# Kernel optimization log

Hardware: AMD Instinct MI355X
Metric: run time of the kernel (lower is better)

## Reference

```python
import jax, jax.numpy as jnp
import numpy as np

HEAD_DIM = 128
N_LAYERS = 32


def setup_inputs() -> dict:
    key = jax.random.key(0)
    kx, kk, kv = jax.random.split(key, 3)
    x = jax.random.normal(kx, (1, 32, 1, HEAD_DIM), dtype=jnp.float32)       # [B,H,1,D] single decode token
    k = jax.random.normal(kk, (1, 32, 8192, HEAD_DIM), dtype=jnp.float32)    # [B,H,S,D] key cache
    v = jax.random.normal(kv, (1, 32, 8192, HEAD_DIM), dtype=jnp.float32)    # [B,H,S,D] value cache
    return {"x": x, "k": k, "v": v}


def _decode_attn(x, k, v):
    # x: [B,H,1,D], k/v: [B,H,S,D]
    scale = 1.0 / np.sqrt(HEAD_DIM).astype(np.float32)
    scores = jnp.einsum("bhqd,bhsd->bhqs", x, k) * scale   # [B,H,1,S]
    probs = jax.nn.softmax(scores, axis=-1)
    return jnp.einsum("bhqs,bhsd->bhqd", probs, v)          # [B,H,1,D]


def reference(x, k, v):
    # gen_id is the (static) cache length; 32 layered decode steps share the cache,
    # mirroring the original loop over 32 layers.
    for _ in range(N_LAYERS):
        x = _decode_attn(x, k, v)
    return (k, v, x)
```

## Files before the change

### kernel.cpp

```cpp
#include <hip/hip_runtime.h>
#include <math.h>

#define HEAD_DIM 128
#define NHEADS   32
#define SLEN     8192
#define NLAYERS  32
#define KROW     (SLEN / 2)
#define VROW     (HEAD_DIM / 2)

#define SPLITS   16
#define CHUNK    (SLEN / SPLITS)
#define PSTR     132
#define SCALE    0.088388347648318447f

typedef unsigned int   uint;
typedef unsigned char  uchar;
typedef __attribute__((ext_vector_type(2))) float f2v;

__device__ __forceinline__ f2v d4_0(uint w) { return __builtin_amdgcn_cvt_scalef32_pk_f32_fp4(w, 1.0f, 0); }
__device__ __forceinline__ f2v d4_1(uint w) { return __builtin_amdgcn_cvt_scalef32_pk_f32_fp4(w, 1.0f, 1); }
__device__ __forceinline__ f2v d4_2(uint w) { return __builtin_amdgcn_cvt_scalef32_pk_f32_fp4(w, 1.0f, 2); }
__device__ __forceinline__ f2v d4_3(uint w) { return __builtin_amdgcn_cvt_scalef32_pk_f32_fp4(w, 1.0f, 3); }

__device__ __forceinline__ uint pk8_fp4(float a0, float a1, float a2, float a3,
                                        float a4, float a5, float a6, float a7) {
    uint r = 0;
    r = __builtin_amdgcn_cvt_scalef32_pk_fp4_f32(r, a0, a1, 1.0f, 0);
    r = __builtin_amdgcn_cvt_scalef32_pk_fp4_f32(r, a2, a3, 1.0f, 1);
    r = __builtin_amdgcn_cvt_scalef32_pk_fp4_f32(r, a4, a5, 1.0f, 2);
    r = __builtin_amdgcn_cvt_scalef32_pk_fp4_f32(r, a6, a7, 1.0f, 3);
    return r;
}

template<bool WRITE_OUT>
__global__ __launch_bounds__(256)
void convert_kT(const float* __restrict__ k, uchar* __restrict__ kbt,
                float* __restrict__ kout)
{
    const int h   = blockIdx.x >> 7;
    const int st  = blockIdx.x & 127;
    const int tid = threadIdx.x;

    __shared__ float tile[HEAD_DIM][65];

    const int   srow0 = tid >> 5;
    const int   c4    = (tid & 31) * 4;
    const size_t kbase = ((size_t)h * SLEN + (size_t)st * 64) * HEAD_DIM;

    #pragma unroll
    for (int it = 0; it < 8; ++it) {
        const int s = srow0 + it * 8;
        const float4 v = *(const float4*)(k + kbase + (size_t)s * HEAD_DIM + c4);
        if (WRITE_OUT) *(float4*)(kout + kbase + (size_t)s * HEAD_DIM + c4) = v;
        tile[c4 + 0][s] = v.x; tile[c4 + 1][s] = v.y;
        tile[c4 + 2][s] = v.z; tile[c4 + 3][s] = v.w;
    }
    __syncthreads();

    const int d0  = tid >> 3;
    const int sl8 = (tid & 7) * 8;
    #pragma unroll
    for (int it = 0; it < 4; ++it) {
        const int d = d0 + it * 32;
        const uint u = pk8_fp4(tile[d][sl8 + 0], tile[d][sl8 + 1],
                               tile[d][sl8 + 2], tile[d][sl8 + 3],
                               tile[d][sl8 + 4], tile[d][sl8 + 5],
                               tile[d][sl8 + 6], tile[d][sl8 + 7]);
        *(uint*)(kbt + ((size_t)h * HEAD_DIM + d) * KROW + st * 32 + (tid & 7) * 4) = u;
    }
}

template<bool WRITE_OUT>
__global__ void convert_v(const float4* __restrict__ v, uint2* __restrict__ vb,
                          float4* __restrict__ vout, size_t n16)
{
    size_t i = (size_t)blockIdx.x * blockDim.x + threadIdx.x;
    const size_t stride = (size_t)gridDim.x * blockDim.x;
    for (size_t j = i; j < n16; j += stride) {
        const float4 b0 = v[4 * j], b1 = v[4 * j + 1], b2 = v[4 * j + 2], b3 = v[4 * j + 3];
        if (WRITE_OUT) {
            vout[4 * j] = b0; vout[4 * j + 1] = b1;
            vout[4 * j + 2] = b2; vout[4 * j + 3] = b3;
        }
        uint2 p;
        p.x = pk8_fp4(b0.x, b0.y, b0.z, b0.w, b1.x, b1.y, b1.z, b1.w);
        p.y = pk8_fp4(b2.x, b2.y, b2.z, b2.w, b3.x, b3.y, b3.z, b3.w);
        vb[j] = p;
    }
}

__global__ void copy_kv(const float4* __restrict__ k, const float4* __restrict__ v,
                        float4* __restrict__ out, size_t n4)
{
    size_t i = (size_t)blockIdx.x * blockDim.x + threadIdx.x;
    const size_t stride = (size_t)gridDim.x * blockDim.x;
    for (size_t j = i; j < n4; j += stride) {
        out[j]      = k[j];
        out[n4 + j] = v[j];
    }
}

__global__ __launch_bounds__(512)
void attn_layer(const float* __restrict__ x0,
                const float* __restrict__ part_in,
                const uchar* __restrict__ kbt,
                const uchar* __restrict__ vb,
                float* __restrict__ part_out)
{
    const int h    = blockIdx.x >> 4;
    const int sp   = blockIdx.x & 15;
    const int tid  = threadIdx.x;
    const int lane = tid & 63;
    const int w    = tid >> 6;

    __shared__ float xs[HEAD_DIM];
    __shared__ float sc[CHUNK];
    __shared__ float scpv[8][HEAD_DIM];
    __shared__ float lred[8];
    __shared__ float xpart[2][HEAD_DIM + 1];
    __shared__ float lpro[2];

    if (part_in) {
        const float* __restrict__ ph = part_in + (size_t)h * SPLITS * PSTR;
        if (tid < 256) {
            const int d = tid & 127, g = tid >> 7;
            float a = 0.f;
            #pragma unroll
            for (int i = 0; i < 8; ++i)
                a += ph[(size_t)(g * 8 + i) * PSTR + 1 + d];
            xpart[g][d] = a;
        } else if (tid < 258) {
            const int g = tid - 256;
            float l = 0.f;
            #pragma unroll
            for (int i = 0; i < 8; ++i)
                l += ph[(size_t)(g * 8 + i) * PSTR];
            lpro[g] = l;
        }
        __syncthreads();
        if (tid < HEAD_DIM)
            xs[tid] = (xpart[0][tid] + xpart[1][tid]) / (lpro[0] + lpro[1]) * SCALE;
    } else {
        if (tid < HEAD_DIM) xs[tid] = x0[h * HEAD_DIM + tid] * SCALE;
    }
    __syncthreads();

    const int sgrp = lane & 3;
    const int dgrp = lane >> 2;
    const uchar* __restrict__ kh = kbt + (size_t)h * HEAD_DIM * KROW + (size_t)sp * (CHUNK / 2);
    const int sboff = w * 32 + sgrp * 8;
    float a16[16];
    #pragma unroll
    for (int j = 0; j < 16; ++j) a16[j] = 0.f;
    #pragma unroll
    for (int it = 0; it < 8; ++it) {
        const int d = it * 16 + dgrp;
        const uint2 kk = *(const uint2*)(kh + (size_t)d * KROW + sboff);
        const float xd = xs[d];
        f2v t;
        t = d4_0(kk.x); a16[0]  = fmaf(t.x, xd, a16[0]);  a16[1]  = fmaf(t.y, xd, a16[1]);
        t = d4_1(kk.x); a16[2]  = fmaf(t.x, xd, a16[2]);  a16[3]  = fmaf(t.y, xd, a16[3]);
        t = d4_2(kk.x); a16[4]  = fmaf(t.x, xd, a16[4]);  a16[5]  = fmaf(t.y, xd, a16[5]);
        t = d4_3(kk.x); a16[6]  = fmaf(t.x, xd, a16[6]);  a16[7]  = fmaf(t.y, xd, a16[7]);
        t = d4_0(kk.y); a16[8]  = fmaf(t.x, xd, a16[8]);  a16[9]  = fmaf(t.y, xd, a16[9]);
        t = d4_1(kk.y); a16[10] = fmaf(t.x, xd, a16[10]); a16[11] = fmaf(t.y, xd, a16[11]);
        t = d4_2(kk.y); a16[12] = fmaf(t.x, xd, a16[12]); a16[13] = fmaf(t.y, xd, a16[13]);
        t = d4_3(kk.y); a16[14] = fmaf(t.x, xd, a16[14]); a16[15] = fmaf(t.y, xd, a16[15]);
    }
    #pragma unroll
    for (int j = 0; j < 16; ++j) {
        a16[j] += __shfl_xor(a16[j], 4);
        a16[j] += __shfl_xor(a16[j], 8);
        a16[j] += __shfl_xor(a16[j], 16);
        a16[j] += __shfl_xor(a16[j], 32);
    }
    float lp = 0.f;
    if (dgrp == 0) {
        const int base = w * 64 + sgrp * 16;
        #pragma unroll
        for (int j = 0; j < 16; ++j) { a16[j] = __expf(a16[j]); lp += a16[j]; }
        #pragma unroll
        for (int j = 0; j < 16; j += 4)
            *(float4*)&sc[base + j] = make_float4(a16[j], a16[j+1], a16[j+2], a16[j+3]);
    }
    #pragma unroll
    for (int off = 1; off < 64; off <<= 1)
        lp += __shfl_xor(lp, off);
    if (lane == 0) lred[w] = lp;
    __syncthreads();

    const int rg = tid >> 3;
    const int dg = tid & 7;
    const uchar* __restrict__ vg = vb + ((size_t)h * SLEN + (size_t)sp * CHUNK) * VROW;
    float acc[16];
    #pragma unroll
    for (int j = 0; j < 16; ++j) acc[j] = 0.f;
    #pragma unroll
    for (int it = 0; it < 8; ++it) {
        const int s1 = rg + it * 64;
        const uint2 vv = *(const uint2*)(vg + (size_t)s1 * VROW + dg * 8);
        const float pp = sc[s1];
        f2v t;
        t = d4_0(vv.x); acc[0]  = fmaf(pp, t.x, acc[0]);  acc[1]  = fmaf(pp, t.y, acc[1]);
        t = d4_1(vv.x); acc[2]  = fmaf(pp, t.x, acc[2]);  acc[3]  = fmaf(pp, t.y, acc[3]);
        t = d4_2(vv.x); acc[4]  = fmaf(pp, t.x, acc[4]);  acc[5]  = fmaf(pp, t.y, acc[5]);
        t = d4_3(vv.x); acc[6]  = fmaf(pp, t.x, acc[6]);  acc[7]  = fmaf(pp, t.y, acc[7]);
        t = d4_0(vv.y); acc[8]  = fmaf(pp, t.x, acc[8]);  acc[9]  = fmaf(pp, t.y, acc[9]);
        t = d4_1(vv.y); acc[10] = fmaf(pp, t.x, acc[10]); acc[11] = fmaf(pp, t.y, acc[11]);
        t = d4_2(vv.y); acc[12] = fmaf(pp, t.x, acc[12]); acc[13] = fmaf(pp, t.y, acc[13]);
        t = d4_3(vv.y); acc[14] = fmaf(pp, t.x, acc[14]); acc[15] = fmaf(pp, t.y, acc[15]);
    }
    #pragma unroll
    for (int j = 0; j < 16; ++j) {
        acc[j] += __shfl_xor(acc[j], 8);
        acc[j] += __shfl_xor(acc[j], 16);
        acc[j] += __shfl_xor(acc[j], 32);
    }
    if (lane < 8) {
        #pragma unroll
        for (int j = 0; j < 16; j += 4)
            *(float4*)&scpv[w][lane * 16 + j] = make_float4(acc[j], acc[j+1], acc[j+2], acc[j+3]);
    }
    __syncthreads();

    float* __restrict__ po = part_out + ((size_t)h * SPLITS + sp) * PSTR;
    if (tid < HEAD_DIM) {
        float a = 0.f;
        #pragma unroll
        for (int g = 0; g < 8; ++g) a += scpv[g][tid];
        po[1 + tid] = a;
    }
    if (tid == 0) {
        float Ls = 0.f;
        #pragma unroll
        for (int i = 0; i < 8; ++i) Ls += lred[i];
        po[0] = Ls;
    }
}

__global__ __launch_bounds__(128)
void attn_combine(const float* __restrict__ part, float* __restrict__ xout)
{
    const float* __restrict__ ph = part + (size_t)blockIdx.x * SPLITS * PSTR;
    float a = 0.f, l = 0.f;
    #pragma unroll
    for (int i = 0; i < SPLITS; ++i) {
        a += ph[(size_t)i * PSTR + 1 + threadIdx.x];
        l += ph[(size_t)i * PSTR];
    }
    xout[blockIdx.x * HEAD_DIM + threadIdx.x] = a / l;
}

extern "C" void kernel_launch(void* const* d_in, const int* in_sizes, int n_in,
                              void* d_out, int out_size, void* d_ws, size_t ws_size,
                              hipStream_t stream)
{
    const float* x = (const float*)d_in[0];
    const float* k = (const float*)d_in[1];
    const float* v = (const float*)d_in[2];
    float* out = (float*)d_out;

    const size_t kvN = (size_t)NHEADS * SLEN * HEAD_DIM;
    const size_t partElems = (size_t)NHEADS * SPLITS * PSTR;

    float* part0 = (float*)d_ws;
    float* part1 = part0 + partElems;

    const size_t needWs = 2 * partElems * sizeof(float) + kvN;
    uchar* kbt;
    uchar* vb;
    const bool ws_path = (ws_size >= needWs + 256);
    if (ws_path) kbt = (uchar*)(part1 + partElems);
    else         kbt = (uchar*)out;
    vb = kbt + kvN / 2;

    if (ws_path) {
        convert_kT<true><<<NHEADS * 128, 256, 0, stream>>>(k, kbt, out);
        convert_v<true><<<2048, 256, 0, stream>>>(
            (const float4*)v, (uint2*)vb, (float4*)(out + kvN), kvN / 16);
    } else {
        convert_kT<false><<<NHEADS * 128, 256, 0, stream>>>(k, kbt, nullptr);
        convert_v<false><<<2048, 256, 0, stream>>>(
            (const float4*)v, (uint2*)vb, nullptr, kvN / 16);
    }

    for (int layer = 0; layer < NLAYERS; ++layer) {
        float* pout = (layer & 1) ? part1 : part0;
        const float* pin = (layer == 0) ? nullptr : ((layer & 1) ? part0 : part1);
        attn_layer<<<NHEADS * SPLITS, 512, 0, stream>>>(
            (layer == 0) ? x : nullptr, pin, kbt, vb, pout);
    }
    attn_combine<<<NHEADS, 128, 0, stream>>>(part1, out + 2 * kvN);

    if (!ws_path) {
        copy_kv<<<2048, 256, 0, stream>>>((const float4*)k, (const float4*)v,
                                          (float4*)out, kvN / 4);
    }
}
```

Baseline: 472.9 us.

## Split QK dot-product across warps by head dim, reduce partial scores in LDS

```diff
diff --git a/kernel.cpp b/kernel.cpp
--- a/kernel.cpp
+++ b/kernel.cpp
@@ -11,6 +11,7 @@
 #define SPLITS   16
 #define CHUNK    (SLEN / SPLITS)
 #define PSTR     132
+#define SCP_STR  20
 #define SCALE    0.088388347648318447f
 
 typedef unsigned int   uint;
@@ -114,6 +115,7 @@
     const int w    = tid >> 6;
 
     __shared__ float xs[HEAD_DIM];
+    __shared__ float scp[8][32 * SCP_STR];
     __shared__ float sc[CHUNK];
     __shared__ float scpv[8][HEAD_DIM];
     __shared__ float lred[8];
@@ -145,17 +147,16 @@
     }
     __syncthreads();
 
-    const int sgrp = lane & 3;
-    const int dgrp = lane >> 2;
+    const int dpar = lane >> 5;
+    const int sgp  = lane & 31;
     const uchar* __restrict__ kh = kbt + (size_t)h * HEAD_DIM * KROW + (size_t)sp * (CHUNK / 2);
-    const int sboff = w * 32 + sgrp * 8;
     float a16[16];
     #pragma unroll
     for (int j = 0; j < 16; ++j) a16[j] = 0.f;
     #pragma unroll
     for (int it = 0; it < 8; ++it) {
-        const int d = it * 16 + dgrp;
-        const uint2 kk = *(const uint2*)(kh + (size_t)d * KROW + sboff);
+        const int d = it * 16 + (w << 1) + dpar;
+        const uint2 kk = *(const uint2*)(kh + (size_t)d * KROW + sgp * 8);
         const float xd = xs[d];
         f2v t;
         t = d4_0(kk.x); a16[0]  = fmaf(t.x, xd, a16[0]);  a16[1]  = fmaf(t.y, xd, a16[1]);
@@ -168,25 +169,25 @@
         t = d4_3(kk.y); a16[14] = fmaf(t.x, xd, a16[14]); a16[15] = fmaf(t.y, xd, a16[15]);
     }
     #pragma unroll
-    for (int j = 0; j < 16; ++j) {
-        a16[j] += __shfl_xor(a16[j], 4);
-        a16[j] += __shfl_xor(a16[j], 8);
-        a16[j] += __shfl_xor(a16[j], 16);
-        a16[j] += __shfl_xor(a16[j], 32);
-    }
-    float lp = 0.f;
-    if (dgrp == 0) {
-        const int base = w * 64 + sgrp * 16;
-        #pragma unroll
-        for (int j = 0; j < 16; ++j) { a16[j] = __expf(a16[j]); lp += a16[j]; }
+    for (int j = 0; j < 16; ++j) a16[j] += __shfl_xor(a16[j], 32);
+    if (lane < 32) {
         #pragma unroll
         for (int j = 0; j < 16; j += 4)
-            *(float4*)&sc[base + j] = make_float4(a16[j], a16[j+1], a16[j+2], a16[j+3]);
-    }
+            *(float4*)&scp[w][sgp * SCP_STR + j] =
+                make_float4(a16[j], a16[j+1], a16[j+2], a16[j+3]);
+    }
+    __syncthreads();
+
+    const int soff = (tid >> 4) * SCP_STR + (tid & 15);
+    const float s = scp[0][soff] + scp[1][soff] + scp[2][soff] + scp[3][soff]
+                  + scp[4][soff] + scp[5][soff] + scp[6][soff] + scp[7][soff];
+    const float e = __expf(s);
+    sc[tid] = e;
+    float l = e;
     #pragma unroll
     for (int off = 1; off < 64; off <<= 1)
-        lp += __shfl_xor(lp, off);
-    if (lane == 0) lred[w] = lp;
+        l += __shfl_xor(l, off);
+    if (lane == 0) lred[w] = l;
     __syncthreads();
 
     const int rg = tid >> 3;
```

New measurement: 398.1 us. -15.8%, faster.
